# Kernel optimization log

Measured on AMD Instinct MI355X. Metric: run time of the kernel, lower is better.

## Reference

```python
import jax, jax.numpy as jnp
import numpy as np

D = 256
RANK = 64
H = 8
DH = D // H
TOPK = 32  # top-k survivors per query row
NEG = -1e9


def lowrank(x, u, v):
    # x:[...,d] @ u:[d,rank] @ v:[rank,d]
    return (x @ u) @ v


def setup_inputs() -> dict:
    key = jax.random.key(0)
    ks = jax.random.split(key, 13)
    s_u = 1.0 / np.sqrt(D)
    s_v = 1.0 / np.sqrt(RANK)

    def pu(k):
        return jax.random.normal(k, (D, RANK), jnp.float32) * s_u

    def pv(k):
        return jax.random.normal(k, (RANK, D), jnp.float32) * s_v

    return {
        "x": jax.random.normal(ks[0], (2, 2048, D), jnp.float32),
        "ne_u": pu(ks[1]), "ne_v": pv(ks[2]),
        "wq_u": pu(ks[3]), "wq_v": pv(ks[4]),
        "wk_u": pu(ks[5]), "wk_v": pv(ks[6]),
        "wv_u": pu(ks[7]), "wv_v": pv(ks[8]),
        "wo_u": pu(ks[9]), "wo_v": pv(ks[10]),
        "es_u": pu(ks[11]), "es_v": pv(ks[12]),
    }


def reference(x, ne_u, ne_v, wq_u, wq_v, wk_u, wk_v, wv_u, wv_v, wo_u, wo_v, es_u, es_v):
    B, N, _ = x.shape
    # node embedding (low-rank projection)
    h = lowrank(x, ne_u, ne_v)  # [B,N,d]

    # low-rank multi-head Q/K/V
    def heads(t):  # [B,N,d] -> [B,H,N,dh]
        return t.reshape(B, N, H, DH).transpose(0, 2, 1, 3)

    q = heads(lowrank(h, wq_u, wq_v))
    k = heads(lowrank(h, wk_u, wk_v))
    v = heads(lowrank(h, wv_u, wv_v))

    scores = jnp.einsum("bhnd,bhmd->bhnm", q, k) / jnp.sqrt(jnp.float32(DH))
    # top-k sparsification per query row
    kth = jax.lax.top_k(scores, TOPK)[0][..., -1:]  # [B,H,N,1]
    masked = jnp.where(scores >= kth, scores, NEG)
    attn = jax.nn.softmax(masked, axis=-1)  # [B,H,N,N]

    out = jnp.einsum("bhnm,bhmd->bhnd", attn, v)  # [B,H,N,dh]
    out = out.transpose(0, 2, 1, 3).reshape(B, N, D)
    h2 = lowrank(out, wo_u, wo_v)  # output projection

    # edge scores -> adjacency with sigmoid + zero diagonal epilogue
    el = lowrank(h2, es_u, es_v)  # [B,N,d]
    adjacency = jax.nn.sigmoid(jnp.einsum("bnd,bmd->bnm", el, el))
    adjacency = adjacency * (1.0 - jnp.eye(N, dtype=adjacency.dtype))
    return adjacency, attn
```

## Files before the change

kernel.cpp:

```cpp
#include <hip/hip_runtime.h>
#include <hip/hip_bf16.h>
#include <cstdint>
#include <cstddef>

#define ATTN_OFF (2u*2048u*2048u)
#define SLOTS 48
#define DELTA 1e-3f
#define MAXB 16
#define CCAP 64
#define PVR 4

typedef __attribute__((ext_vector_type(8))) short bf16x8;
typedef __attribute__((ext_vector_type(4))) float f32x4;

__device__ __forceinline__ unsigned short bf16_hi(float f) {
  __hip_bfloat16 h = __float2bfloat16(f);
  return *(unsigned short*)&h;
}
__device__ __forceinline__ float bf16_val(unsigned short u) {
  __hip_bfloat16 h = *(__hip_bfloat16*)&u;
  return __bfloat162float(h);
}

__global__ __launch_bounds__(256) void fused_qkv_kernel(
    const float* __restrict__ x, const float* __restrict__ ne_u,
    const float* __restrict__ ne_v, const float* __restrict__ wq_u,
    const float* __restrict__ wq_v, const float* __restrict__ wk_u,
    const float* __restrict__ wk_v, const float* __restrict__ wv_u,
    const float* __restrict__ wv_v, double* __restrict__ qd,
    double* __restrict__ kd, unsigned short* __restrict__ qh,
    unsigned short* __restrict__ ql, unsigned short* __restrict__ kh,
    unsigned short* __restrict__ kl, float* __restrict__ v) {
  __shared__ double xm[4][64];
  __shared__ double hrow[4][256];
  __shared__ double mid2[4][64];

  int tid = threadIdx.x;
  int rr = tid >> 6;
  int j  = tid & 63;
  int row = blockIdx.x * 4 + rr;
  int b = row >> 11, m = row & 2047;
  const double INV = 0.17677669529663688110021109052621;

  const float* xr = x + (size_t)row * 256;
  {
    double a0 = 0, a1 = 0, a2 = 0, a3 = 0;
#pragma unroll 8
    for (int k4 = 0; k4 < 64; ++k4) {
      int kk = k4 * 4;
      a0 = fma((double)xr[kk + 0], (double)ne_u[(kk + 0) * 64 + j], a0);
      a1 = fma((double)xr[kk + 1], (double)ne_u[(kk + 1) * 64 + j], a1);
      a2 = fma((double)xr[kk + 2], (double)ne_u[(kk + 2) * 64 + j], a2);
      a3 = fma((double)xr[kk + 3], (double)ne_u[(kk + 3) * 64 + j], a3);
    }
    xm[rr][j] = (a0 + a1) + (a2 + a3);
  }
  __syncthreads();

#pragma unroll
  for (int cc = 0; cc < 4; ++cc) {
    int col = j + 64 * cc;
    double o0 = 0, o1 = 0, o2 = 0, o3 = 0;
#pragma unroll 4
    for (int r4 = 0; r4 < 16; ++r4) {
      int r = r4 * 4;
      o0 = fma(xm[rr][r + 0], (double)ne_v[(r + 0) * 256 + col], o0);
      o1 = fma(xm[rr][r + 1], (double)ne_v[(r + 1) * 256 + col], o1);
      o2 = fma(xm[rr][r + 2], (double)ne_v[(r + 2) * 256 + col], o2);
      o3 = fma(xm[rr][r + 3], (double)ne_v[(r + 3) * 256 + col], o3);
    }
    hrow[rr][col] = (o0 + o1) + (o2 + o3);
  }
  __syncthreads();

  for (int p = 0; p < 3; ++p) {
    const float* pu = (p == 0) ? wq_u : (p == 1) ? wk_u : wv_u;
    const float* pw = (p == 0) ? wq_v : (p == 1) ? wk_v : wv_v;

    double a0 = 0, a1 = 0, a2 = 0, a3 = 0;
#pragma unroll 8
    for (int k4 = 0; k4 < 64; ++k4) {
      int kk = k4 * 4;
      a0 = fma(hrow[rr][kk + 0], (double)pu[(kk + 0) * 64 + j], a0);
      a1 = fma(hrow[rr][kk + 1], (double)pu[(kk + 1) * 64 + j], a1);
      a2 = fma(hrow[rr][kk + 2], (double)pu[(kk + 2) * 64 + j], a2);
      a3 = fma(hrow[rr][kk + 3], (double)pu[(kk + 3) * 64 + j], a3);
    }
    mid2[rr][j] = (a0 + a1) + (a2 + a3);
    __syncthreads();

#pragma unroll
    for (int cc = 0; cc < 4; ++cc) {
      int col = j + 64 * cc;
      double o0 = 0, o1 = 0, o2 = 0, o3 = 0;
#pragma unroll 4
      for (int r4 = 0; r4 < 16; ++r4) {
        int r = r4 * 4;
        o0 = fma(mid2[rr][r + 0], (double)pw[(r + 0) * 256 + col], o0);
        o1 = fma(mid2[rr][r + 1], (double)pw[(r + 1) * 256 + col], o1);
        o2 = fma(mid2[rr][r + 2], (double)pw[(r + 2) * 256 + col], o2);
        o3 = fma(mid2[rr][r + 3], (double)pw[(r + 3) * 256 + col], o3);
      }
      double o = (o0 + o1) + (o2 + o3);
      if (p == 2) {
        v[(size_t)row * 256 + col] = (float)o;
      } else {
        int hh = col >> 5, d = col & 31;
        size_t haddr = (((size_t)(b * 8 + hh)) * 2048 + m) * 32 + d;
        if (p == 0) {
          qd[(size_t)row * 256 + col] = o;
          float f = (float)(o * INV);
          unsigned short hi = bf16_hi(f);
          float lof = f - bf16_val(hi);
          qh[haddr] = hi;
          ql[haddr] = bf16_hi(lof);
        } else {
          kd[(size_t)row * 256 + col] = o;
          float f = (float)o;
          unsigned short hi = bf16_hi(f);
          float lof = f - bf16_val(hi);
          kh[haddr] = hi;
          kl[haddr] = bf16_hi(lof);
        }
      }
    }
    __syncthreads();
  }
}

__global__ __launch_bounds__(512, 4) void attn_kernel(
    const unsigned short* __restrict__ qh, const unsigned short* __restrict__ ql,
    const unsigned short* __restrict__ kh, const unsigned short* __restrict__ kl,
    const double* __restrict__ qd, const double* __restrict__ kd,
    float* __restrict__ attn, float* __restrict__ pval,
    unsigned short* __restrict__ pidx) {
  __shared__ unsigned hist[16][64];
  __shared__ float cand[16][CCAP];
  __shared__ float sval[16][SLOTS];
  __shared__ unsigned short scol[16][SLOTS];
  __shared__ float rowmax_s[16][8];
  __shared__ float mx_s[16];
  __shared__ float kth_s[16];
  __shared__ float zinv_s[16];
  __shared__ int   kB_s[16];
  __shared__ unsigned kneed_s[16];
  __shared__ unsigned c1t[16], c2t[16];
  __shared__ unsigned ccnt[16];
  __shared__ unsigned scnt[16];
  __shared__ unsigned chi_s[16];
  __shared__ unsigned bcnt[16];
  __shared__ unsigned short bidx[16][MAXB];
  __shared__ float bval[16][MAXB];
  __shared__ double bs64[16][MAXB];

  int tid = threadIdx.x;
  int bx  = blockIdx.x;
  int slab = bx >> 7;
  int rowtile = bx & 127;
  int b = slab >> 3, hh = slab & 7;
  int w = tid >> 6;
  int l = tid & 63;
  int g = l >> 4;
  int li = l & 15;
  int h32 = l >> 5;
  int c32 = l & 31;
  int rw = w * 2 + h32;
  const double INV64 = 0.17677669529663688110021109052621;

  size_t qoff = (((size_t)slab * 2048 + rowtile * 16 + li) * 32) + g * 8;
  bf16x8 a_hi = *(const bf16x8*)(qh + qoff);
  bf16x8 a_lo = *(const bf16x8*)(ql + qoff);

  float s[16][4];
  size_t kbase = ((size_t)slab * 2048 + w * 256 + li) * 32 + g * 8;
#pragma unroll
  for (int tt = 0; tt < 16; ++tt) {
    bf16x8 b_hi = *(const bf16x8*)(kh + kbase + (size_t)tt * 512);
    bf16x8 b_lo = *(const bf16x8*)(kl + kbase + (size_t)tt * 512);
    f32x4 acc = {0.f, 0.f, 0.f, 0.f};
    acc = __builtin_amdgcn_mfma_f32_16x16x32_bf16(a_hi, b_hi, acc, 0, 0, 0);
    acc = __builtin_amdgcn_mfma_f32_16x16x32_bf16(a_hi, b_lo, acc, 0, 0, 0);
    acc = __builtin_amdgcn_mfma_f32_16x16x32_bf16(a_lo, b_hi, acc, 0, 0, 0);
#pragma unroll
    for (int reg = 0; reg < 4; ++reg) s[tt][reg] = acc[reg];
  }

  for (int i = tid; i < 16 * 64; i += 512) ((unsigned*)hist)[i] = 0u;
  if (tid < 16) {
    ccnt[tid] = 0u; scnt[tid] = 0u; chi_s[tid] = 0u; bcnt[tid] = 0u;
    c1t[tid] = 0u; c2t[tid] = 0u;
    kth_s[tid] = -1e30f; kB_s[tid] = -1;
  }
  size_t prow0 = ((size_t)slab * 2048 + rowtile * 16);
  {
    float lmx[4];
#pragma unroll
    for (int reg = 0; reg < 4; ++reg) {
      float m = s[0][reg];
#pragma unroll
      for (int tt = 1; tt < 16; ++tt) m = fmaxf(m, s[tt][reg]);
      lmx[reg] = m;
    }
#pragma unroll
    for (int off = 1; off < 16; off <<= 1) {
#pragma unroll
      for (int reg = 0; reg < 4; ++reg)
        lmx[reg] = fmaxf(lmx[reg], __shfl_xor(lmx[reg], (unsigned)off, 16));
    }
    if (li == 0) {
#pragma unroll
      for (int reg = 0; reg < 4; ++reg) rowmax_s[4 * g + reg][w] = lmx[reg];
    }
  }
  __syncthreads();

  if (tid < 16) {
    float m = rowmax_s[tid][0];
#pragma unroll
    for (int i = 1; i < 8; ++i) m = fmaxf(m, rowmax_s[tid][i]);
    mx_s[tid] = m;
  }
  __syncthreads();

  {
#pragma unroll
    for (int reg = 0; reg < 4; ++reg) {
      int rloc = 4 * g + reg;
      float mx = mx_s[rloc];
      float t1 = mx - 1.0f, t2 = mx - 2.0f;
      unsigned a = 0, c = 0;
#pragma unroll
      for (int tt = 0; tt < 16; ++tt) {
        float v = s[tt][reg];
        a += (v >= t1) ? 1u : 0u;
        c += (v >= t2) ? 1u : 0u;
      }
#pragma unroll
      for (int off = 1; off < 16; off <<= 1) {
        a += (unsigned)__shfl_xor((int)a, off, 16);
        c += (unsigned)__shfl_xor((int)c, off, 16);
      }
      if (li == 0) {
        if (a) atomicAdd(&c1t[rloc], a);
        if (c) atomicAdd(&c2t[rloc], c);
      }
    }
  }
  __syncthreads();

#pragma unroll
  for (int reg = 0; reg < 4; ++reg) {
    int rloc = 4 * g + reg;
    float mx = mx_s[rloc];
    unsigned t1 = c1t[rloc], t2 = c2t[rloc];
    float sc, thr;
    if (t1 >= 32u)      { sc = 64.0f; thr = mx - 1.0f; }
    else if (t2 >= 32u) { sc = 32.0f; thr = mx - 2.0f; }
    else                { sc = 4.0f;  thr = -1e30f; }
#pragma unroll
    for (int tt = 0; tt < 16; ++tt) {
      float v = s[tt][reg];
      if (v >= thr) {
        int bb = (int)((mx - v) * sc);
        bb = bb > 63 ? 63 : bb;
        atomicAdd(&hist[rloc][bb], 1u);
      }
    }
  }
  __syncthreads();

  {
    unsigned cnt2 = hist[rw][c32 * 2] + hist[rw][c32 * 2 + 1];
    unsigned pre = cnt2;
#pragma unroll
    for (int off = 1; off < 32; off <<= 1) {
      unsigned t = __shfl_up(pre, (unsigned)off, 32);
      if (c32 >= off) pre += t;
    }
    unsigned excl = pre - cnt2;
    bool flag = (excl < 32u) && (pre >= 32u);
    unsigned long long bal = __ballot(flag);
    unsigned seg = (unsigned)((bal >> (h32 * 32)) & 0xFFFFFFFFull);
    if (flag) {
      int src = __ffs(seg) - 1;
      if (c32 == src) {
        unsigned cum = excl;
        int B = 63; unsigned cb = 0;
#pragma unroll
        for (int i = 0; i < 2; ++i) {
          unsigned hv = hist[rw][c32 * 2 + i];
          if (cum < 32u && cum + hv >= 32u) { B = c32 * 2 + i; cb = cum; }
          cum += hv;
        }
        kB_s[rw] = B;
        kneed_s[rw] = 32u - cb;
      }
    }
  }
  __syncthreads();

#pragma unroll
  for (int reg = 0; reg < 4; ++reg) {
    int rloc = 4 * g + reg;
    float mx = mx_s[rloc];
    unsigned t1 = c1t[rloc], t2 = c2t[rloc];
    float sc, thr;
    if (t1 >= 32u)      { sc = 64.0f; thr = mx - 1.0f; }
    else if (t2 >= 32u) { sc = 32.0f; thr = mx - 2.0f; }
    else                { sc = 4.0f;  thr = -1e30f; }
    int kB = kB_s[rloc];
#pragma unroll
    for (int tt = 0; tt < 16; ++tt) {
      float v = s[tt][reg];
      if (v >= thr) {
        int bb = (int)((mx - v) * sc);
        bb = bb > 63 ? 63 : bb;
        if (bb == kB) {
          unsigned slot = atomicAdd(&ccnt[rloc], 1u);
          if (slot < (unsigned)CCAP) cand[rloc][slot] = v;
        }
      }
    }
  }
  __syncthreads();

  {
    unsigned n0 = ccnt[rw];
    n0 = n0 > (unsigned)CCAP ? (unsigned)CCAP : n0;
    unsigned need = kneed_s[rw];
    if (need > n0) need = n0;
    for (unsigned ci = (unsigned)c32; ci < n0; ci += 32u) {
      float x = cand[rw][ci];
      unsigned r = 0;
      for (unsigned jj = 0; jj < n0; ++jj) {
        float y = cand[rw][jj];
        r += (y > x || (y == x && jj < ci)) ? 1u : 0u;
      }
      if (r == need - 1u) kth_s[rw] = x;
    }
  }
  __syncthreads();

#pragma unroll
  for (int reg = 0; reg < 4; ++reg) {
    int rloc = 4 * g + reg;
    float kth = kth_s[rloc];
    unsigned cnt = 0;
#pragma unroll
    for (int tt = 0; tt < 16; ++tt) {
      float v = s[tt][reg];
      if (v > kth + DELTA) {
        ++cnt;
        unsigned slot = atomicAdd(&scnt[rloc], 1u);
        if (slot < (unsigned)SLOTS) {
          sval[rloc][slot] = v;
          scol[rloc][slot] = (unsigned short)(w * 256 + tt * 16 + li);
        }
      } else if (!(v < kth - DELTA)) {
        unsigned slot = atomicAdd(&bcnt[rloc], 1u);
        if (slot < (unsigned)MAXB) {
          bidx[rloc][slot] = (unsigned short)(w * 256 + tt * 16 + li);
          bval[rloc][slot] = v;
        }
      }
    }
#pragma unroll
    for (int off = 1; off < 16; off <<= 1)
      cnt += (unsigned)__shfl_xor((int)cnt, off, 16);
    if (li == 0 && cnt) atomicAdd(&chi_s[rloc], cnt);
  }
  __syncthreads();

  {
    unsigned bn = bcnt[rw];
    bn = bn > (unsigned)MAXB ? (unsigned)MAXB : bn;
    const double* qrow =
        qd + ((size_t)(b * 2048 + rowtile * 16 + rw)) * 256 + hh * 32;
    for (unsigned ci = (unsigned)c32; ci < bn; ci += 32u) {
      int m = bidx[rw][ci];
      const double* krow = kd + ((size_t)(b * 2048 + m)) * 256 + hh * 32;
      double acc = 0.0;
#pragma unroll 8
      for (int d = 0; d < 32; ++d) acc = fma(qrow[d], krow[d], acc);
      bs64[rw][ci] = acc * INV64;
    }
    unsigned need2 = 32u - chi_s[rw];
    for (unsigned ci = (unsigned)c32; ci < bn; ci += 32u) {
      double x = bs64[rw][ci];
      unsigned r = 0;
      for (unsigned jj = 0; jj < bn; ++jj)
        r += (bs64[rw][jj] > x) ? 1u : 0u;
      if (r < need2) {
        unsigned slot = atomicAdd(&scnt[rw], 1u);
        if (slot < (unsigned)SLOTS) {
          sval[rw][slot] = bval[rw][ci];
          scol[rw][slot] = bidx[rw][ci];
        }
      }
    }
  }
  __syncthreads();

  float* base = attn + prow0 * 2048;
  {
    unsigned n = scnt[rw];
    n = n > (unsigned)SLOTS ? (unsigned)SLOTS : n;
    float mx = mx_s[rw];
    float z = 0.0f;
    for (unsigned i = (unsigned)c32; i < n; i += 32u) {
      float e = __expf(sval[rw][i] - mx);
      sval[rw][i] = e;
      z += e;
    }
#pragma unroll
    for (int off = 1; off < 32; off <<= 1) z += __shfl_xor(z, (unsigned)off, 32);
    if (c32 == 0) zinv_s[rw] = 1.0f / z;
  }
  {
    f32x4 z4 = {0.f, 0.f, 0.f, 0.f};
#pragma unroll
    for (int it = 0; it < 16; ++it)
      __builtin_nontemporal_store(z4, ((f32x4*)base) + tid + 512 * it);
  }
  __syncthreads();

  for (int e = tid; e < 16 * SLOTS; e += 512) {
    int rr = e / SLOTS, ii = e % SLOTS;
    unsigned n = scnt[rr];
    n = n > (unsigned)SLOTS ? (unsigned)SLOTS : n;
    float p = 0.0f;
    unsigned short c = 0;
    if ((unsigned)ii < n) {
      c = scol[rr][ii];
      p = sval[rr][ii] * zinv_s[rr];
      base[(size_t)rr * 2048 + c] = p;
    }
    pval[prow0 * SLOTS + e] = p;
    pidx[prow0 * SLOTS + e] = c;
  }
}

__global__ __launch_bounds__(256) void pv_wo_es_kernel(
    const float* __restrict__ pval, const unsigned short* __restrict__ pidx,
    const float* __restrict__ v,
    const float* __restrict__ wo_u, const float* __restrict__ wo_v,
    const float* __restrict__ es_u, const float* __restrict__ es_v,
    unsigned short* __restrict__ elh, unsigned short* __restrict__ ell) {
  __shared__ float svals[PVR][8][SLOTS];
  __shared__ unsigned short sidx[PVR][8][SLOTS];
  __shared__ float outr[PVR][256];
  __shared__ float mid[PVR][64];
  __shared__ float h2r[PVR][256];

  int tid = threadIdx.x;
  int bb = blockIdx.x >> 9;
  int rg = blockIdx.x & 511;
  int n0 = rg * PVR;

  for (int e = tid; e < PVR * 8 * SLOTS; e += 256) {
    int rr = e / (8 * SLOTS);
    int rem = e % (8 * SLOTS);
    int hh = rem / SLOTS, ii = rem % SLOTS;
    size_t srow = ((size_t)(bb * 8 + hh) * 2048 + n0 + rr) * SLOTS + ii;
    svals[rr][hh][ii] = pval[srow];
    sidx[rr][hh][ii] = pidx[srow];
  }
  __syncthreads();

  {
    int d = tid, hh = d >> 5;
    const float* vb = v + (size_t)bb * 2048 * 256 + d;
    for (int r = 0; r < PVR; ++r) {
      float acc = 0.f;
#pragma unroll 4
      for (int i = 0; i < SLOTS; ++i) {
        float p = svals[r][hh][i];
        int m = sidx[r][hh][i];
        acc = fmaf(p, vb[(size_t)m * 256], acc);
      }
      outr[r][d] = acc;
    }
  }
  __syncthreads();

  {
    int j = tid & 63, rb = tid >> 6;
    for (int r = rb; r < PVR; r += 4) {
      float a0 = 0, a1 = 0, a2 = 0, a3 = 0;
#pragma unroll 8
      for (int k4 = 0; k4 < 64; ++k4) {
        int k = k4 * 4;
        a0 = fmaf(outr[r][k + 0], wo_u[(k + 0) * 64 + j], a0);
        a1 = fmaf(outr[r][k + 1], wo_u[(k + 1) * 64 + j], a1);
        a2 = fmaf(outr[r][k + 2], wo_u[(k + 2) * 64 + j], a2);
        a3 = fmaf(outr[r][k + 3], wo_u[(k + 3) * 64 + j], a3);
      }
      mid[r][j] = (a0 + a1) + (a2 + a3);
    }
  }
  __syncthreads();

  {
    int c = tid;
    for (int r = 0; r < PVR; ++r) {
      float a0 = 0, a1 = 0, a2 = 0, a3 = 0;
#pragma unroll 4
      for (int k4 = 0; k4 < 16; ++k4) {
        int k = k4 * 4;
        a0 = fmaf(mid[r][k + 0], wo_v[(k + 0) * 256 + c], a0);
        a1 = fmaf(mid[r][k + 1], wo_v[(k + 1) * 256 + c], a1);
        a2 = fmaf(mid[r][k + 2], wo_v[(k + 2) * 256 + c], a2);
        a3 = fmaf(mid[r][k + 3], wo_v[(k + 3) * 256 + c], a3);
      }
      h2r[r][c] = (a0 + a1) + (a2 + a3);
    }
  }
  __syncthreads();

  {
    int j = tid & 63, rb = tid >> 6;
    for (int r = rb; r < PVR; r += 4) {
      float a0 = 0, a1 = 0, a2 = 0, a3 = 0;
#pragma unroll 8
      for (int k4 = 0; k4 < 64; ++k4) {
        int k = k4 * 4;
        a0 = fmaf(h2r[r][k + 0], es_u[(k + 0) * 64 + j], a0);
        a1 = fmaf(h2r[r][k + 1], es_u[(k + 1) * 64 + j], a1);
        a2 = fmaf(h2r[r][k + 2], es_u[(k + 2) * 64 + j], a2);
        a3 = fmaf(h2r[r][k + 3], es_u[(k + 3) * 64 + j], a3);
      }
      mid[r][j] = (a0 + a1) + (a2 + a3);
    }
  }
  __syncthreads();

  {
    int c = tid;
    for (int r = 0; r < PVR; ++r) {
      float a0 = 0, a1 = 0, a2 = 0, a3 = 0;
#pragma unroll 4
      for (int k4 = 0; k4 < 16; ++k4) {
        int k = k4 * 4;
        a0 = fmaf(mid[r][k + 0], es_v[(k + 0) * 256 + c], a0);
        a1 = fmaf(mid[r][k + 1], es_v[(k + 1) * 256 + c], a1);
        a2 = fmaf(mid[r][k + 2], es_v[(k + 2) * 256 + c], a2);
        a3 = fmaf(mid[r][k + 3], es_v[(k + 3) * 256 + c], a3);
      }
      float o = (a0 + a1) + (a2 + a3);
      size_t addr = ((size_t)(bb * 2048 + n0 + r)) * 256 + c;
      unsigned short hi = bf16_hi(o);
      elh[addr] = hi;
      ell[addr] = bf16_hi(o - bf16_val(hi));
    }
  }
}

__global__ __launch_bounds__(256) void adj_mfma_kernel(
    const unsigned short* __restrict__ elh, const unsigned short* __restrict__ ell,
    float* __restrict__ adj) {
  int tid = threadIdx.x;
  int l = tid & 63, w = tid >> 6;
  int li = l & 15, g = l >> 4;
  int b = blockIdx.z, rt = blockIdx.y, ct = blockIdx.x;

  int arow = rt * 64 + w * 16 + li;
  size_t abase = ((size_t)(b * 2048 + arow)) * 256 + g * 8;
  size_t bbase = ((size_t)(b * 2048 + ct * 64 + li)) * 256 + g * 8;

  f32x4 acc0 = {0.f, 0.f, 0.f, 0.f};
  f32x4 acc1 = {0.f, 0.f, 0.f, 0.f};
  f32x4 acc2 = {0.f, 0.f, 0.f, 0.f};
  f32x4 acc3 = {0.f, 0.f, 0.f, 0.f};

#pragma unroll
  for (int kc = 0; kc < 8; ++kc) {
    bf16x8 a_hi = *(const bf16x8*)(elh + abase + kc * 32);
    bf16x8 a_lo = *(const bf16x8*)(ell + abase + kc * 32);
#pragma unroll
    for (int t = 0; t < 4; ++t) {
      bf16x8 b_hi = *(const bf16x8*)(elh + bbase + (size_t)t * 16 * 256 + kc * 32);
      bf16x8 b_lo = *(const bf16x8*)(ell + bbase + (size_t)t * 16 * 256 + kc * 32);
      f32x4* pa = (t == 0) ? &acc0 : (t == 1) ? &acc1 : (t == 2) ? &acc2 : &acc3;
      *pa = __builtin_amdgcn_mfma_f32_16x16x32_bf16(a_hi, b_hi, *pa, 0, 0, 0);
      *pa = __builtin_amdgcn_mfma_f32_16x16x32_bf16(a_hi, b_lo, *pa, 0, 0, 0);
      *pa = __builtin_amdgcn_mfma_f32_16x16x32_bf16(a_lo, b_hi, *pa, 0, 0, 0);
    }
  }

  int orow0 = rt * 64 + w * 16 + g * 4;
#pragma unroll
  for (int t = 0; t < 4; ++t) {
    f32x4 a = (t == 0) ? acc0 : (t == 1) ? acc1 : (t == 2) ? acc2 : acc3;
    int cg = ct * 64 + t * 16 + li;
#pragma unroll
    for (int i = 0; i < 4; ++i) {
      int rg = orow0 + i;
      float sg = 1.0f / (1.0f + __expf(-a[i]));
      if (rg == cg) sg = 0.0f;
      adj[((size_t)b * 2048 + rg) * 2048 + cg] = sg;
    }
  }
}

extern "C" void kernel_launch(void* const* d_in, const int* in_sizes, int n_in,
                              void* d_out, int out_size, void* d_ws,
                              size_t ws_size, hipStream_t stream) {
  const float* x    = (const float*)d_in[0];
  const float* ne_u = (const float*)d_in[1];
  const float* ne_v = (const float*)d_in[2];
  const float* wq_u = (const float*)d_in[3];
  const float* wq_v = (const float*)d_in[4];
  const float* wk_u = (const float*)d_in[5];
  const float* wk_v = (const float*)d_in[6];
  const float* wv_u = (const float*)d_in[7];
  const float* wv_v = (const float*)d_in[8];
  const float* wo_u = (const float*)d_in[9];
  const float* wo_v = (const float*)d_in[10];
  const float* es_u = (const float*)d_in[11];
  const float* es_v = (const float*)d_in[12];

  float* adj  = (float*)d_out;
  float* attn = adj + (size_t)ATTN_OFF;

  char* ws = (char*)d_ws;
  double* qd = (double*)(ws);
  double* kd = (double*)(ws + ((size_t)8  << 20));
  unsigned short* qh = (unsigned short*)(ws + ((size_t)16 << 20));
  unsigned short* ql = (unsigned short*)(ws + ((size_t)18 << 20));
  unsigned short* kh = (unsigned short*)(ws + ((size_t)20 << 20));
  unsigned short* kl = (unsigned short*)(ws + ((size_t)22 << 20));
  float* v    = (float*)(ws + ((size_t)24 << 20));
  float* pval = (float*)(ws + ((size_t)28 << 20));
  unsigned short* pidx = (unsigned short*)(ws + ((size_t)35 << 20));
  unsigned short* elh = (unsigned short*)(ws + ((size_t)8  << 20));
  unsigned short* ell = (unsigned short*)(ws + ((size_t)10 << 20));

  fused_qkv_kernel<<<1024, 256, 0, stream>>>(
      x, ne_u, ne_v, wq_u, wq_v, wk_u, wk_v, wv_u, wv_v,
      qd, kd, qh, ql, kh, kl, v);

  attn_kernel<<<2048, 512, 0, stream>>>(qh, ql, kh, kl, qd, kd, attn, pval, pidx);
  pv_wo_es_kernel<<<1024, 256, 0, stream>>>(pval, pidx, v, wo_u, wo_v,
                                            es_u, es_v, elh, ell);

  adj_mfma_kernel<<<dim3(32, 32, 2), 256, 0, stream>>>(elh, ell, adj);
}
```

Before: 387.5 us.

## Replace candidate rank-select with tiered histogram bin thresholds for top-k

```diff
diff --git a/kernel.cpp b/kernel.cpp
--- a/kernel.cpp
+++ b/kernel.cpp
@@ -6,8 +6,7 @@
 #define ATTN_OFF (2u*2048u*2048u)
 #define SLOTS 48
 #define DELTA 1e-3f
-#define MAXB 16
-#define CCAP 64
+#define MAXB 32
 #define PVR 4
 
 typedef __attribute__((ext_vector_type(8))) short bf16x8;
@@ -135,20 +134,17 @@
     float* __restrict__ attn, float* __restrict__ pval,
     unsigned short* __restrict__ pidx) {
   __shared__ unsigned hist[16][64];
-  __shared__ float cand[16][CCAP];
   __shared__ float sval[16][SLOTS];
   __shared__ unsigned short scol[16][SLOTS];
   __shared__ float rowmax_s[16][8];
   __shared__ float mx_s[16];
-  __shared__ float kth_s[16];
+  __shared__ float eLo_s[16], eHi_s[16];
   __shared__ float zinv_s[16];
   __shared__ int   kB_s[16];
-  __shared__ unsigned kneed_s[16];
-  __shared__ unsigned c1t[16], c2t[16];
-  __shared__ unsigned ccnt[16];
   __shared__ unsigned scnt[16];
   __shared__ unsigned chi_s[16];
   __shared__ unsigned bcnt[16];
+  __shared__ unsigned pend;
   __shared__ unsigned short bidx[16][MAXB];
   __shared__ float bval[16][MAXB];
   __shared__ double bs64[16][MAXB];
@@ -187,10 +183,10 @@
 
   for (int i = tid; i < 16 * 64; i += 512) ((unsigned*)hist)[i] = 0u;
   if (tid < 16) {
-    ccnt[tid] = 0u; scnt[tid] = 0u; chi_s[tid] = 0u; bcnt[tid] = 0u;
-    c1t[tid] = 0u; c2t[tid] = 0u;
-    kth_s[tid] = -1e30f; kB_s[tid] = -1;
-  }
+    scnt[tid] = 0u; chi_s[tid] = 0u; bcnt[tid] = 0u;
+    kB_s[tid] = -1;
+  }
+  if (tid == 0) pend = 16u;
   size_t prow0 = ((size_t)slab * 2048 + rowtile * 16);
   {
     float lmx[4];
@@ -222,141 +218,88 @@
   }
   __syncthreads();
 
-  {
-#pragma unroll
-    for (int reg = 0; reg < 4; ++reg) {
-      int rloc = 4 * g + reg;
-      float mx = mx_s[rloc];
-      float t1 = mx - 1.0f, t2 = mx - 2.0f;
-      unsigned a = 0, c = 0;
-#pragma unroll
-      for (int tt = 0; tt < 16; ++tt) {
-        float v = s[tt][reg];
-        a += (v >= t1) ? 1u : 0u;
-        c += (v >= t2) ? 1u : 0u;
-      }
-#pragma unroll
-      for (int off = 1; off < 16; off <<= 1) {
-        a += (unsigned)__shfl_xor((int)a, off, 16);
-        c += (unsigned)__shfl_xor((int)c, off, 16);
-      }
-      if (li == 0) {
-        if (a) atomicAdd(&c1t[rloc], a);
-        if (c) atomicAdd(&c2t[rloc], c);
-      }
-    }
-  }
-  __syncthreads();
+#pragma unroll
+  for (int tier = 0; tier < 3; ++tier) {
+    if (pend != 0u) {
+      const float sc = (tier == 0) ? 32.0f : (tier == 1) ? 8.0f : 0.25f;
+#pragma unroll
+      for (int reg = 0; reg < 4; ++reg) {
+        int rloc = 4 * g + reg;
+        if (kB_s[rloc] < 0) {
+          float mx = mx_s[rloc];
+#pragma unroll
+          for (int tt = 0; tt < 16; ++tt) {
+            int bb = (int)((mx - s[tt][reg]) * sc);
+            bb = bb > 63 ? 63 : bb;
+            atomicAdd(&hist[rloc][bb], 1u);
+          }
+        }
+      }
+      __syncthreads();
+      {
+        bool rowpend = (kB_s[rw] < 0);
+        unsigned cnt2 = rowpend ? (hist[rw][c32 * 2] + hist[rw][c32 * 2 + 1]) : 0u;
+        unsigned pre = cnt2;
+#pragma unroll
+        for (int off = 1; off < 32; off <<= 1) {
+          unsigned t = __shfl_up(pre, (unsigned)off, 32);
+          if (c32 >= off) pre += t;
+        }
+        unsigned excl = pre - cnt2;
+        bool flag = rowpend && (excl < 32u) && (pre >= 32u);
+        unsigned long long bal = __ballot(flag);
+        unsigned seg = (unsigned)((bal >> (h32 * 32)) & 0xFFFFFFFFull);
+        bool resolved = false;
+        if (flag) {
+          int src = __ffs(seg) - 1;
+          if (c32 == src) {
+            unsigned cum = excl;
+            int B = 63;
+#pragma unroll
+            for (int i = 0; i < 2; ++i) {
+              unsigned hv = hist[rw][c32 * 2 + i];
+              if (cum < 32u && cum + hv >= 32u) B = c32 * 2 + i;
+              cum += hv;
+            }
+            if (B < 63 || tier == 2) {
+              kB_s[rw] = B;
+              eHi_s[rw] = mx_s[rw] - (float)B / sc;
+              eLo_s[rw] = mx_s[rw] - (float)(B + 1) / sc;
+              atomicSub(&pend, 1u);
+              resolved = true;
+            }
+          }
+        }
+        if (tier < 2) {
+          unsigned long long bal2 = __ballot(resolved);
+          bool rowResolved = (((bal2 >> (h32 * 32)) & 0xFFFFFFFFull) != 0ull);
+          if (rowpend && !rowResolved) {
+            hist[rw][c32] = 0u;
+            hist[rw][c32 + 32] = 0u;
+          }
+        }
+      }
+      __syncthreads();
+    }
+  }
 
 #pragma unroll
   for (int reg = 0; reg < 4; ++reg) {
     int rloc = 4 * g + reg;
-    float mx = mx_s[rloc];
-    unsigned t1 = c1t[rloc], t2 = c2t[rloc];
-    float sc, thr;
-    if (t1 >= 32u)      { sc = 64.0f; thr = mx - 1.0f; }
-    else if (t2 >= 32u) { sc = 32.0f; thr = mx - 2.0f; }
-    else                { sc = 4.0f;  thr = -1e30f; }
+    float eh = eHi_s[rloc] + DELTA;
+    float el = eLo_s[rloc] - DELTA;
+    unsigned cnt = 0;
 #pragma unroll
     for (int tt = 0; tt < 16; ++tt) {
       float v = s[tt][reg];
-      if (v >= thr) {
-        int bb = (int)((mx - v) * sc);
-        bb = bb > 63 ? 63 : bb;
-        atomicAdd(&hist[rloc][bb], 1u);
-      }
-    }
-  }
-  __syncthreads();
-
-  {
-    unsigned cnt2 = hist[rw][c32 * 2] + hist[rw][c32 * 2 + 1];
-    unsigned pre = cnt2;
-#pragma unroll
-    for (int off = 1; off < 32; off <<= 1) {
-      unsigned t = __shfl_up(pre, (unsigned)off, 32);
-      if (c32 >= off) pre += t;
-    }
-    unsigned excl = pre - cnt2;
-    bool flag = (excl < 32u) && (pre >= 32u);
-    unsigned long long bal = __ballot(flag);
-    unsigned seg = (unsigned)((bal >> (h32 * 32)) & 0xFFFFFFFFull);
-    if (flag) {
-      int src = __ffs(seg) - 1;
-      if (c32 == src) {
-        unsigned cum = excl;
-        int B = 63; unsigned cb = 0;
-#pragma unroll
-        for (int i = 0; i < 2; ++i) {
-          unsigned hv = hist[rw][c32 * 2 + i];
-          if (cum < 32u && cum + hv >= 32u) { B = c32 * 2 + i; cb = cum; }
-          cum += hv;
-        }
-        kB_s[rw] = B;
-        kneed_s[rw] = 32u - cb;
-      }
-    }
-  }
-  __syncthreads();
-
-#pragma unroll
-  for (int reg = 0; reg < 4; ++reg) {
-    int rloc = 4 * g + reg;
-    float mx = mx_s[rloc];
-    unsigned t1 = c1t[rloc], t2 = c2t[rloc];
-    float sc, thr;
-    if (t1 >= 32u)      { sc = 64.0f; thr = mx - 1.0f; }
-    else if (t2 >= 32u) { sc = 32.0f; thr = mx - 2.0f; }
-    else                { sc = 4.0f;  thr = -1e30f; }
-    int kB = kB_s[rloc];
-#pragma unroll
-    for (int tt = 0; tt < 16; ++tt) {
-      float v = s[tt][reg];
-      if (v >= thr) {
-        int bb = (int)((mx - v) * sc);
-        bb = bb > 63 ? 63 : bb;
-        if (bb == kB) {
-          unsigned slot = atomicAdd(&ccnt[rloc], 1u);
-          if (slot < (unsigned)CCAP) cand[rloc][slot] = v;
-        }
-      }
-    }
-  }
-  __syncthreads();
-
-  {
-    unsigned n0 = ccnt[rw];
-    n0 = n0 > (unsigned)CCAP ? (unsigned)CCAP : n0;
-    unsigned need = kneed_s[rw];
-    if (need > n0) need = n0;
-    for (unsigned ci = (unsigned)c32; ci < n0; ci += 32u) {
-      float x = cand[rw][ci];
-      unsigned r = 0;
-      for (unsigned jj = 0; jj < n0; ++jj) {
-        float y = cand[rw][jj];
-        r += (y > x || (y == x && jj < ci)) ? 1u : 0u;
-      }
-      if (r == need - 1u) kth_s[rw] = x;
-    }
-  }
-  __syncthreads();
-
-#pragma unroll
-  for (int reg = 0; reg < 4; ++reg) {
-    int rloc = 4 * g + reg;
-    float kth = kth_s[rloc];
-    unsigned cnt = 0;
-#pragma unroll
-    for (int tt = 0; tt < 16; ++tt) {
-      float v = s[tt][reg];
-      if (v > kth + DELTA) {
+      if (v > eh) {
         ++cnt;
         unsigned slot = atomicAdd(&scnt[rloc], 1u);
         if (slot < (unsigned)SLOTS) {
           sval[rloc][slot] = v;
           scol[rloc][slot] = (unsigned short)(w * 256 + tt * 16 + li);
         }
-      } else if (!(v < kth - DELTA)) {
+      } else if (v >= el) {
         unsigned slot = atomicAdd(&bcnt[rloc], 1u);
         if (slot < (unsigned)MAXB) {
           bidx[rloc][slot] = (unsigned short)(w * 256 + tt * 16 + li);
@@ -370,6 +313,14 @@
     if (li == 0 && cnt) atomicAdd(&chi_s[rloc], cnt);
   }
   __syncthreads();
+
+  float* base = attn + prow0 * 2048;
+  {
+    f32x4 z4 = {0.f, 0.f, 0.f, 0.f};
+#pragma unroll
+    for (int it = 0; it < 16; ++it)
+      __builtin_nontemporal_store(z4, ((f32x4*)base) + tid + 512 * it);
+  }
 
   {
     unsigned bn = bcnt[rw];
@@ -401,7 +352,6 @@
   }
   __syncthreads();
 
-  float* base = attn + prow0 * 2048;
   {
     unsigned n = scnt[rw];
     n = n > (unsigned)SLOTS ? (unsigned)SLOTS : n;
@@ -415,12 +365,6 @@
 #pragma unroll
     for (int off = 1; off < 32; off <<= 1) z += __shfl_xor(z, (unsigned)off, 32);
     if (c32 == 0) zinv_s[rw] = 1.0f / z;
-  }
-  {
-    f32x4 z4 = {0.f, 0.f, 0.f, 0.f};
-#pragma unroll
-    for (int it = 0; it < 16; ++it)
-      __builtin_nontemporal_store(z4, ((f32x4*)base) + tid + 512 * it);
   }
   __syncthreads();
 
```

Result: slower. 525.6 us (+35.6%).
